# Optimization experiments

Measured on AMD Instinct MI355X. Metric: run time of the kernel, lower is better.

Reference implementation:

```python
import jax, jax.numpy as jnp
import numpy as np
from jax import lax

VOCAB, D, LAYERS, PAD = 10000, 200, 3, 3
B, S = 16, 512
SCALE = 0.05  # ~ torch uniform(-1/sqrt(200), 1/sqrt(200)) scale


def setup_inputs() -> dict:
    key = jax.random.key(0)
    ks = jax.random.split(key, 8)
    x = jax.random.randint(ks[0], (B, S), 0, VOCAB)
    emb = jax.random.normal(ks[1], (VOCAB, D), jnp.float32) * SCALE
    emb = emb.at[PAD].set(0.0)  # padding_idx=3 row is zeros
    w_ih = jax.random.normal(ks[2], (LAYERS, D, D), jnp.float32) * SCALE
    w_hh = jax.random.normal(ks[3], (LAYERS, D, D), jnp.float32) * SCALE
    b_ih = jax.random.normal(ks[4], (LAYERS, D), jnp.float32) * SCALE
    b_hh = jax.random.normal(ks[5], (LAYERS, D), jnp.float32) * SCALE
    fc_w = jax.random.normal(ks[6], (VOCAB, D), jnp.float32) * SCALE
    fc_b = jax.random.normal(ks[7], (VOCAB,), jnp.float32) * SCALE
    return {"x": x, "emb": emb, "w_ih": w_ih, "w_hh": w_hh,
            "b_ih": b_ih, "b_hh": b_hh, "fc_w": fc_w, "fc_b": fc_b}


def _rnn_forward(x, emb, w_ih, w_hh, b_ih, b_hh, fc_w, fc_b):
    h = emb[x]  # (B, S, D) embedding gather
    finals = []
    for l in range(LAYERS):
        # precompute input projection for the whole sequence (efficient GEMM)
        xw = jnp.einsum('bsd,hd->bsh', h, w_ih[l]) + b_ih[l] + b_hh[l]  # (B,S,D)
        w_hh_l_T = w_hh[l].T

        def step(h_prev, x_t):
            h_new = jnp.tanh(x_t + h_prev @ w_hh_l_T)
            return h_new, h_new

        h0 = jnp.zeros((x.shape[0], D), xw.dtype)
        h_last, outs = lax.scan(step, h0, jnp.swapaxes(xw, 0, 1))  # scan over time
        h = jnp.swapaxes(outs, 0, 1)  # (B, S, D)
        finals.append(h_last)
    hidden = jnp.stack(finals)  # (LAYERS, B, D) like torch RNN hidden
    logits = h @ fc_w.T + fc_b  # (B, S, VOCAB)
    return logits, hidden


def reference(x, emb, w_ih, w_hh, b_ih, b_hh, fc_w, fc_b):
    # forward always starts from zero hidden (source ignores the hidden arg)
    return _rnn_forward(x, emb, w_ih, w_hh, b_ih, b_hh, fc_w, fc_b)
```

## Files before the change

### kernel.cpp

```cpp
#include <hip/hip_runtime.h>
#include <hip/hip_bf16.h>

#define VOCAB 10000
#define D 200
#define NLAYERS 3
#define NB 16
#define NS 512
#define M 8192
#define KA 224
#define KB 232
#define NPADA 10120
#define NTILES_N 79

#define OFF_BUF0 0u
#define OFF_BUF1 6553600u
#define OFF_WT   13107200u
#define OFF_HBF  13587200u
#define OFF_FWB  17257216u
#define OFF_STG1 21952896u
#define WS_NEED  28506496u

typedef __bf16 bf16x8 __attribute__((ext_vector_type(8)));
typedef float  f32x4  __attribute__((ext_vector_type(4)));
typedef unsigned int u32x4 __attribute__((ext_vector_type(4)));

__global__ void k_embed(const int* __restrict__ x, const float* __restrict__ emb,
                        float* __restrict__ h0) {
    int i = blockIdx.x * blockDim.x + threadIdx.x;
    if (i < M * D) {
        int bs = i / D;
        int d  = i - bs * D;
        h0[i] = emb[(size_t)x[bs] * D + d];
    }
}

__global__ void k_wtrans(const float* __restrict__ w_ih, float* __restrict__ wt) {
    int i = blockIdx.x * blockDim.x + threadIdx.x;
    if (i < NLAYERS * D * D) {
        int l = i / (D * D);
        int r = i - l * D * D;
        int k = r / D;
        int n = r - k * D;
        wt[i] = w_ih[l * D * D + n * D + k];
    }
}

__global__ void k_fcwbf(const float* __restrict__ fc_w, __bf16* __restrict__ fwb) {
    int i = blockIdx.x * blockDim.x + threadIdx.x;
    if (i < NPADA * KB) {
        int n = i / KB;
        int k = i - n * KB;
        float v = (n < VOCAB && k < D) ? fc_w[(size_t)n * D + k] : 0.f;
        fwb[i] = (__bf16)v;
    }
}

__global__ void k_hbf2(const float* __restrict__ h, __bf16* __restrict__ hbf) {
    int i = blockIdx.x * blockDim.x + threadIdx.x;
    if (i < M * KA) {
        int m = i / KA;
        int k = i - m * KA;
        float v = (k < D) ? h[(size_t)m * D + k] : 0.f;
        hbf[i] = (__bf16)v;
    }
}

__global__ void k_zero(u32x4* __restrict__ p, int n4) {
    int i = blockIdx.x * blockDim.x + threadIdx.x;
    if (i < n4) p[i] = u32x4{0u, 0u, 0u, 0u};
}

__global__ void k_xw(const float* __restrict__ hin, const float* __restrict__ wt,
                     const float* __restrict__ b_ih, const float* __restrict__ b_hh,
                     float* __restrict__ xw) {
    int m0 = blockIdx.x * 32;
    int n  = threadIdx.x;
    if (n >= D) return;
    float bias = b_ih[n] + b_hh[n];
    for (int g = 0; g < 8; ++g) {
        const float* r0 = hin + (size_t)(m0 + g * 4) * D;
        float a0 = bias, a1 = bias, a2 = bias, a3 = bias;
        for (int k = 0; k < D; k += 4) {
            #pragma unroll
            for (int kk = 0; kk < 4; ++kk) {
                float w = wt[(k + kk) * D + n];
                float h0v = r0[k + kk];
                float h1v = r0[D + k + kk];
                float h2v = r0[2 * D + k + kk];
                float h3v = r0[3 * D + k + kk];
                a0 += h0v * w; a1 += h1v * w; a2 += h2v * w; a3 += h3v * w;
            }
        }
        size_t o = (size_t)(m0 + g * 4) * D + n;
        xw[o] = a0; xw[o + D] = a1; xw[o + 2 * D] = a2; xw[o + 3 * D] = a3;
    }
}

__device__ inline float fast_tanh(float x) {
    x = fminf(fmaxf(x, -15.f), 15.f);
    float e = __expf(2.f * x);
    return (e - 1.f) / (e + 1.f);
}

__global__ __attribute__((amdgpu_flat_work_group_size(512, 512),
                          amdgpu_waves_per_eu(2, 2)))
void k_scan_pipe(const float* __restrict__ whh_all,
                 const float* __restrict__ wih_all,
                 const float* __restrict__ b_ih,
                 const float* __restrict__ b_hh,
                 const float* __restrict__ xw0,
                 unsigned* __restrict__ stage0,
                 unsigned* __restrict__ stage1,
                 __bf16* __restrict__ hbf,
                 float* __restrict__ hidden) {
    __shared__ float hp0[208], hp1[208], hin[208];
    const int bid = blockIdx.x;
    const int l   = bid >> 4;
    const int b   = bid & 15;
    const int t   = threadIdx.x;
    const int q   = t >> 2, dg = t & 3;
    const bool act = (q < 100);
    const int  rr  = 2 * q + (dg & 1);
    const int  rrl = act ? rr : 0;
    const bool wlane = act && (dg < 2);
    const int  dstart = dg * 52;

    f32x4 wh[2][13], wi[2][13];
    #pragma unroll
    for (int j = 0; j < 2; ++j)
        #pragma unroll
        for (int i = 0; i < 13; ++i) {
            wh[j][i] = f32x4{0.f, 0.f, 0.f, 0.f};
            wi[j][i] = f32x4{0.f, 0.f, 0.f, 0.f};
        }
    if (act) {
        #pragma unroll
        for (int j = 0; j < 2; ++j) {
            const float* wr = whh_all + (size_t)l * D * D + (size_t)(2 * q + j) * D + dstart;
            #pragma unroll
            for (int i = 0; i < 11; ++i) wh[j][i] = *(const f32x4*)(wr + 4 * i);
            if (dg < 3) {
                wh[j][11] = *(const f32x4*)(wr + 44);
                wh[j][12] = *(const f32x4*)(wr + 48);
            }
        }
        if (l > 0) {
            #pragma unroll
            for (int j = 0; j < 2; ++j) {
                const float* wr = wih_all + (size_t)l * D * D + (size_t)(2 * q + j) * D + dstart;
                #pragma unroll
                for (int i = 0; i < 11; ++i) wi[j][i] = *(const f32x4*)(wr + 4 * i);
                if (dg < 3) {
                    wi[j][11] = *(const f32x4*)(wr + 44);
                    wi[j][12] = *(const f32x4*)(wr + 48);
                }
            }
        }
    }
    float bias = 0.f;
    if (l > 0 && act) bias = b_ih[l * D + rr] + b_hh[l * D + rr];

    if (t < 208) { hp0[t] = 0.f; hp1[t] = 0.f; hin[t] = 0.f; }
    __syncthreads();

    const float* xrow = xw0 + (size_t)b * NS * D;
    const unsigned* sin = (l == 1) ? stage0 + (size_t)b * NS * 200
                        : (l == 2) ? stage1 + (size_t)b * NS * 200 : nullptr;
    unsigned* sout = (l == 0) ? stage0 + (size_t)b * NS * 200
                   : (l == 1) ? stage1 + (size_t)b * NS * 200 : nullptr;

    float xv_next = (l == 0) ? xrow[rrl] : 0.f;
    float hlast = 0.f;
    const float* hi = hin + dstart;

    #pragma unroll 1
    for (int s = 0; s < NS; ++s) {
        float xv;
        if (l == 0) {
            xv = xv_next;
            const int sn = (s + 1 < NS) ? s + 1 : NS - 1;
            xv_next = xrow[(size_t)sn * D + rrl];
        } else {
            if (t < 200) {
                const unsigned* p = sin + (size_t)s * 200 + t;
                unsigned v;
                do {
                    v = __hip_atomic_load(p, __ATOMIC_RELAXED,
                                          __HIP_MEMORY_SCOPE_AGENT);
                } while (v == 0u);
                hin[t] = __builtin_bit_cast(float, ~v);
            }
            asm volatile("s_waitcnt lgkmcnt(0)" ::: "memory");
            __builtin_amdgcn_s_barrier();
            asm volatile("" ::: "memory");
            xv = bias;
        }
        const float* hr = ((s & 1) ? hp1 : hp0) + dstart;
        float* hw = (s & 1) ? hp0 : hp1;
        f32x4 ac0{0.f,0.f,0.f,0.f}, ac1{0.f,0.f,0.f,0.f};
        #pragma unroll
        for (int i = 0; i < 13; ++i) {
            f32x4 h4 = *(const f32x4*)(hr + 4 * i);
            ac0 += h4 * wh[0][i];
            ac1 += h4 * wh[1][i];
        }
        if (l > 0) {
            #pragma unroll
            for (int i = 0; i < 13; ++i) {
                f32x4 g4 = *(const f32x4*)(hi + 4 * i);
                ac0 += g4 * wi[0][i];
                ac1 += g4 * wi[1][i];
            }
        }
        float s0 = (ac0.x + ac0.y) + (ac0.z + ac0.w);
        float s1 = (ac1.x + ac1.y) + (ac1.z + ac1.w);
        s0 += __shfl_xor(s0, 1);  s0 += __shfl_xor(s0, 2);
        s1 += __shfl_xor(s1, 1);  s1 += __shfl_xor(s1, 2);
        float hn = fast_tanh(xv + ((dg & 1) ? s1 : s0));
        hlast = hn;
        if (wlane) {
            hw[rr] = hn;
            if (l < 2) {
                __hip_atomic_store(sout + (size_t)s * 200 + rr,
                                   ~__builtin_bit_cast(unsigned, hn),
                                   __ATOMIC_RELAXED, __HIP_MEMORY_SCOPE_AGENT);
            } else {
                hbf[((size_t)b * NS + s) * KA + rr] = (__bf16)hn;
            }
        }
        asm volatile("s_waitcnt lgkmcnt(0)" ::: "memory");
        __builtin_amdgcn_s_barrier();
        asm volatile("" ::: "memory");
    }
    if (wlane) hidden[(size_t)l * NB * D + b * D + rr] = hlast;
}

#define STEP(HR, HW, SIDX)                                                  \
    {                                                                       \
        float xv = xv_next;                                                 \
        int snext = (SIDX) + 1 < NS ? (SIDX) + 1 : NS - 1;                  \
        xv_next = xrow[(size_t)snext * D + rrl];                            \
        f32x4 ac0{0.f,0.f,0.f,0.f}, ac1{0.f,0.f,0.f,0.f};                   \
        _Pragma("unroll")                                                   \
        for (int i = 0; i < 13; ++i) {                                      \
            f32x4 h4 = *(const f32x4*)((HR) + 4 * i);                       \
            ac0 += h4 * w4[0][i];                                           \
            ac1 += h4 * w4[1][i];                                           \
        }                                                                   \
        float s0 = (ac0.x + ac0.y) + (ac0.z + ac0.w);                       \
        float s1 = (ac1.x + ac1.y) + (ac1.z + ac1.w);                       \
        s0 += __shfl_xor(s0, 1);  s0 += __shfl_xor(s0, 2);                  \
        s1 += __shfl_xor(s1, 1);  s1 += __shfl_xor(s1, 2);                  \
        float hn = fast_tanh(xv + ((dg & 1) ? s1 : s0));                    \
        hlast = hn;                                                         \
        if (wlane) {                                                        \
            (HW)[rr] = hn;                                                  \
            xrow[(size_t)(SIDX) * D + rr] = hn;                             \
        }                                                                   \
        __syncthreads();                                                    \
    }

__global__ __attribute__((amdgpu_flat_work_group_size(512, 512),
                          amdgpu_waves_per_eu(2, 2)))
void k_scan(const float* __restrict__ whh,
            float* __restrict__ io,
            float* __restrict__ hidden) {
    __shared__ float hp0[208], hp1[208];
    int t  = threadIdx.x;
    int b  = blockIdx.x;
    int q  = t >> 2;
    int dg = t & 3;
    const bool act = (q < 100);
    const int  rr  = 2 * q + (dg & 1);
    const int  rrl = act ? rr : 0;
    const bool wlane = act && (dg < 2);
    const int  dstart = dg * 52;

    f32x4 w4[2][13];
    #pragma unroll
    for (int j = 0; j < 2; ++j)
        #pragma unroll
        for (int i = 0; i < 13; ++i) w4[j][i] = f32x4{0.f, 0.f, 0.f, 0.f};
    if (act) {
        #pragma unroll
        for (int j = 0; j < 2; ++j) {
            const float* wr = whh + (size_t)(2 * q + j) * D + dstart;
            #pragma unroll
            for (int i = 0; i < 11; ++i) w4[j][i] = *(const f32x4*)(wr + 4 * i);
            if (dg < 3) {
                w4[j][11] = *(const f32x4*)(wr + 44);
                w4[j][12] = *(const f32x4*)(wr + 48);
            }
        }
    }
    if (t < 208) { hp0[t] = 0.f; hp1[t] = 0.f; }
    __syncthreads();

    float* xrow = io + (size_t)b * NS * D;
    const float* hr0 = hp0 + dstart;
    const float* hr1 = hp1 + dstart;
    float xv_next = xrow[rrl];
    float hlast = 0.f;

    #pragma unroll 1
    for (int s2 = 0; s2 < NS / 2; ++s2) {
        STEP(hr0, hp1, 2 * s2)
        STEP(hr1, hp0, 2 * s2 + 1)
    }
    if (wlane) hidden[b * D + rr] = hlast;
}

__global__ __launch_bounds__(256) void k_fc(const __bf16* __restrict__ A,
                                            const __bf16* __restrict__ Bw,
                                            const float* __restrict__ fc_b,
                                            float* __restrict__ Cout) {
    __shared__ __bf16 Bl[3840 * 8];
    int tid = threadIdx.x;
    int wg  = blockIdx.x;
    int mt  = wg / NTILES_N, nt = wg - mt * NTILES_N;
    int m0  = mt * 128, n0 = nt * 128;

    {
        const u32x4* src = (const u32x4*)(Bw + (size_t)n0 * KB);
        u32x4* dst = (u32x4*)Bl;
        u32x4 stg[15];
        #pragma unroll
        for (int it = 0; it < 15; ++it) stg[it] = src[tid + it * 256];
        #pragma unroll
        for (int it = 0; it < 15; ++it) dst[tid + it * 256] = stg[it];
    }
    __syncthreads();

    int lane = tid & 63, wv = tid >> 6;
    int wr = wv >> 1, wc = wv & 1;
    int lr = lane & 15, lq = lane >> 4;
    f32x4 acc[4][4] = {};
    #pragma unroll
    for (int ks = 0; ks < 7; ++ks) {
        bf16x8 af[4], bfr[4];
        #pragma unroll
        for (int i = 0; i < 4; ++i) {
            int arow = m0 + wr * 64 + i * 16 + lr;
            af[i] = *(const bf16x8*)(A + (size_t)arow * KA + (ks * 4 + lq) * 8);
            int brow = wc * 64 + i * 16 + lr;
            bfr[i] = *(const bf16x8*)(Bl + brow * KB + (ks * 4 + lq) * 8);
        }
        #pragma unroll
        for (int i = 0; i < 4; ++i) {
            #pragma unroll
            for (int j = 0; j < 4; ++j) {
                acc[i][j] = __builtin_amdgcn_mfma_f32_16x16x32_bf16(af[i], bfr[j],
                                                                   acc[i][j], 0, 0, 0);
            }
        }
    }
    #pragma unroll
    for (int j = 0; j < 4; ++j) {
        int col = n0 + wc * 64 + j * 16 + lr;
        if (col < VOCAB) {
            float bias = fc_b[col];
            #pragma unroll
            for (int i = 0; i < 4; ++i) {
                #pragma unroll
                for (int r = 0; r < 4; ++r) {
                    int row = m0 + wr * 64 + i * 16 + lq * 4 + r;
                    Cout[(size_t)row * VOCAB + col] = acc[i][j][r] + bias;
                }
            }
        }
    }
}

extern "C" void kernel_launch(void* const* d_in, const int* in_sizes, int n_in,
                              void* d_out, int out_size, void* d_ws, size_t ws_size,
                              hipStream_t stream) {
    const int*   x    = (const int*)  d_in[0];
    const float* emb  = (const float*)d_in[1];
    const float* w_ih = (const float*)d_in[2];
    const float* w_hh = (const float*)d_in[3];
    const float* b_ih = (const float*)d_in[4];
    const float* b_hh = (const float*)d_in[5];
    const float* fc_w = (const float*)d_in[6];
    const float* fc_b = (const float*)d_in[7];
    float* out    = (float*)d_out;
    float* hidden = out + (size_t)M * VOCAB;

    char* ws = (char*)d_ws;
    float*    buf0 = (float*)(ws + OFF_BUF0);
    float*    buf1 = (float*)(ws + OFF_BUF1);
    float*    wt   = (float*)(ws + OFF_WT);
    __bf16*   hbf  = (__bf16*)(ws + OFF_HBF);
    __bf16*   fwb  = (__bf16*)(ws + OFF_FWB);
    unsigned* stg0 = (unsigned*)(ws + OFF_BUF0);
    unsigned* stg1 = (unsigned*)(ws + OFF_STG1);

    k_embed <<<(M * D + 255) / 256, 256, 0, stream>>>(x, emb, buf0);
    k_wtrans<<<(NLAYERS * D * D + 255) / 256, 256, 0, stream>>>(w_ih, wt);
    k_fcwbf <<<(NPADA * KB + 255) / 256, 256, 0, stream>>>(fc_w, fwb);

    if (ws_size >= WS_NEED) {
        k_xw<<<M / 32, 256, 0, stream>>>(buf0, wt, b_ih, b_hh, buf1);
        const int nst4 = NB * NS * 200 / 4;
        const int nhb4 = M * KA * 2 / 16;
        k_zero<<<(nst4 + 255) / 256, 256, 0, stream>>>((u32x4*)stg0, nst4);
        k_zero<<<(nst4 + 255) / 256, 256, 0, stream>>>((u32x4*)stg1, nst4);
        k_zero<<<(nhb4 + 255) / 256, 256, 0, stream>>>((u32x4*)hbf, nhb4);
        k_scan_pipe<<<NB * NLAYERS, 512, 0, stream>>>(w_hh, w_ih, b_ih, b_hh,
                                                      buf1, stg0, stg1, hbf, hidden);
    } else {
        float* cur = buf0;
        float* nxt = buf1;
        for (int l = 0; l < NLAYERS; ++l) {
            k_xw  <<<M / 32, 256, 0, stream>>>(cur, wt + l * D * D,
                                               b_ih + l * D, b_hh + l * D, nxt);
            k_scan<<<NB, 512, 0, stream>>>(w_hh + (size_t)l * D * D, nxt,
                                           hidden + l * NB * D);
            float* tswap = cur; cur = nxt; nxt = tswap;
        }
        k_hbf2<<<(M * KA + 255) / 256, 256, 0, stream>>>(cur, hbf);
    }
    k_fc<<<64 * NTILES_N, 256, 0, stream>>>(hbf, fwb, fc_b, out);
}
```

Measured before the change: 866.7 us.

## Compute next layer's input projection in producer block, remove per-step input barrier

Each layer block now multiplies its freshly computed hidden state by the next layer's W_ih (plus bias) and publishes the projected value per row, instead of publishing raw h for the consumer to project. Consumer layers then only need one scalar per output row from the staging buffer, and they prefetch it one step ahead. This removes the separate LDS staging of the input vector and the extra barrier per timestep in consumer blocks. The cost is extra FMAs and registers in the producer's serial critical path. The loop also gains one extra iteration to drain the final projection.

```diff
diff --git a/kernel.cpp b/kernel.cpp
--- a/kernel.cpp
+++ b/kernel.cpp
@@ -109,11 +109,11 @@
                  const float* __restrict__ b_ih,
                  const float* __restrict__ b_hh,
                  const float* __restrict__ xw0,
-                 unsigned* __restrict__ stage0,
-                 unsigned* __restrict__ stage1,
+                 unsigned* __restrict__ cells1,
+                 unsigned* __restrict__ cells2,
                  __bf16* __restrict__ hbf,
                  float* __restrict__ hidden) {
-    __shared__ float hp0[208], hp1[208], hin[208];
+    __shared__ float hp0[208], hp1[208];
     const int bid = blockIdx.x;
     const int l   = bid >> 4;
     const int b   = bid & 15;
@@ -125,13 +125,13 @@
     const bool wlane = act && (dg < 2);
     const int  dstart = dg * 52;
 
-    f32x4 wh[2][13], wi[2][13];
+    f32x4 wh[2][13], wp[2][13];
     #pragma unroll
     for (int j = 0; j < 2; ++j)
         #pragma unroll
         for (int i = 0; i < 13; ++i) {
             wh[j][i] = f32x4{0.f, 0.f, 0.f, 0.f};
-            wi[j][i] = f32x4{0.f, 0.f, 0.f, 0.f};
+            wp[j][i] = f32x4{0.f, 0.f, 0.f, 0.f};
         }
     if (act) {
         #pragma unroll
@@ -144,95 +144,111 @@
                 wh[j][12] = *(const f32x4*)(wr + 48);
             }
         }
-        if (l > 0) {
+        if (l < 2) {
             #pragma unroll
             for (int j = 0; j < 2; ++j) {
-                const float* wr = wih_all + (size_t)l * D * D + (size_t)(2 * q + j) * D + dstart;
+                const float* wr = wih_all + (size_t)(l + 1) * D * D + (size_t)(2 * q + j) * D + dstart;
                 #pragma unroll
-                for (int i = 0; i < 11; ++i) wi[j][i] = *(const f32x4*)(wr + 4 * i);
+                for (int i = 0; i < 11; ++i) wp[j][i] = *(const f32x4*)(wr + 4 * i);
                 if (dg < 3) {
-                    wi[j][11] = *(const f32x4*)(wr + 44);
-                    wi[j][12] = *(const f32x4*)(wr + 48);
+                    wp[j][11] = *(const f32x4*)(wr + 44);
+                    wp[j][12] = *(const f32x4*)(wr + 48);
                 }
             }
         }
     }
-    float bias = 0.f;
-    if (l > 0 && act) bias = b_ih[l * D + rr] + b_hh[l * D + rr];
-
-    if (t < 208) { hp0[t] = 0.f; hp1[t] = 0.f; hin[t] = 0.f; }
+    float bN = 0.f;
+    if (l < 2 && act) bN = b_ih[(l + 1) * D + rr] + b_hh[(l + 1) * D + rr];
+
+    if (t < 208) { hp0[t] = 0.f; hp1[t] = 0.f; }
     __syncthreads();
 
     const float* xrow = xw0 + (size_t)b * NS * D;
-    const unsigned* sin = (l == 1) ? stage0 + (size_t)b * NS * 200
-                        : (l == 2) ? stage1 + (size_t)b * NS * 200 : nullptr;
-    unsigned* sout = (l == 0) ? stage0 + (size_t)b * NS * 200
-                   : (l == 1) ? stage1 + (size_t)b * NS * 200 : nullptr;
-
-    float xv_next = (l == 0) ? xrow[rrl] : 0.f;
-    float hlast = 0.f;
-    const float* hi = hin + dstart;
+    const unsigned* cin = (l == 1) ? cells1 + (size_t)b * NS * 200
+                        : (l == 2) ? cells2 + (size_t)b * NS * 200 : nullptr;
+    unsigned* cout_ = (l == 0) ? cells1 + (size_t)b * NS * 200
+                    : (l == 1) ? cells2 + (size_t)b * NS * 200 : nullptr;
+
+    float hn_prev = 0.f;
+    float xv_cur = 0.f;
+    unsigned v_cur = 0u;
+    if (l == 0) xv_cur = xrow[rrl];
 
     #pragma unroll 1
-    for (int s = 0; s < NS; ++s) {
-        float xv;
-        if (l == 0) {
-            xv = xv_next;
-            const int sn = (s + 1 < NS) ? s + 1 : NS - 1;
-            xv_next = xrow[(size_t)sn * D + rrl];
-        } else {
-            if (t < 200) {
-                const unsigned* p = sin + (size_t)s * 200 + t;
-                unsigned v;
-                do {
-                    v = __hip_atomic_load(p, __ATOMIC_RELAXED,
-                                          __HIP_MEMORY_SCOPE_AGENT);
-                } while (v == 0u);
-                hin[t] = __builtin_bit_cast(float, ~v);
-            }
-            asm volatile("s_waitcnt lgkmcnt(0)" ::: "memory");
-            __builtin_amdgcn_s_barrier();
-            asm volatile("" ::: "memory");
-            xv = bias;
-        }
-        const float* hr = ((s & 1) ? hp1 : hp0) + dstart;
-        float* hw = (s & 1) ? hp0 : hp1;
-        f32x4 ac0{0.f,0.f,0.f,0.f}, ac1{0.f,0.f,0.f,0.f};
-        #pragma unroll
-        for (int i = 0; i < 13; ++i) {
-            f32x4 h4 = *(const f32x4*)(hr + 4 * i);
-            ac0 += h4 * wh[0][i];
-            ac1 += h4 * wh[1][i];
-        }
-        if (l > 0) {
-            #pragma unroll
-            for (int i = 0; i < 13; ++i) {
-                f32x4 g4 = *(const f32x4*)(hi + 4 * i);
-                ac0 += g4 * wi[0][i];
-                ac1 += g4 * wi[1][i];
-            }
-        }
-        float s0 = (ac0.x + ac0.y) + (ac0.z + ac0.w);
-        float s1 = (ac1.x + ac1.y) + (ac1.z + ac1.w);
-        s0 += __shfl_xor(s0, 1);  s0 += __shfl_xor(s0, 2);
-        s1 += __shfl_xor(s1, 1);  s1 += __shfl_xor(s1, 2);
-        float hn = fast_tanh(xv + ((dg & 1) ? s1 : s0));
-        hlast = hn;
-        if (wlane) {
-            hw[rr] = hn;
-            if (l < 2) {
-                __hip_atomic_store(sout + (size_t)s * 200 + rr,
-                                   ~__builtin_bit_cast(unsigned, hn),
-                                   __ATOMIC_RELAXED, __HIP_MEMORY_SCOPE_AGENT);
-            } else {
-                hbf[((size_t)b * NS + s) * KA + rr] = (__bf16)hn;
-            }
-        }
+    for (int s = 0; s <= NS; ++s) {
+        float* hw = (s & 1) ? hp1 : hp0;
+        if (wlane) hw[rr] = hn_prev;
         asm volatile("s_waitcnt lgkmcnt(0)" ::: "memory");
         __builtin_amdgcn_s_barrier();
         asm volatile("" ::: "memory");
-    }
-    if (wlane) hidden[(size_t)l * NB * D + b * D + rr] = hlast;
+        const float* hr = hw + dstart;
+
+        f32x4 a0{0.f,0.f,0.f,0.f}, a1{0.f,0.f,0.f,0.f};
+        f32x4 p0{0.f,0.f,0.f,0.f}, p1{0.f,0.f,0.f,0.f};
+        if (l < 2) {
+            #pragma unroll
+            for (int i = 0; i < 13; ++i) {
+                f32x4 h4 = *(const f32x4*)(hr + 4 * i);
+                a0 += h4 * wh[0][i];
+                a1 += h4 * wh[1][i];
+                p0 += h4 * wp[0][i];
+                p1 += h4 * wp[1][i];
+            }
+        } else {
+            #pragma unroll
+            for (int i = 0; i < 13; ++i) {
+                f32x4 h4 = *(const f32x4*)(hr + 4 * i);
+                a0 += h4 * wh[0][i];
+                a1 += h4 * wh[1][i];
+            }
+        }
+
+        if (l < 2 && s >= 1) {
+            float t0 = (p0.x + p0.y) + (p0.z + p0.w);
+            float t1 = (p1.x + p1.y) + (p1.z + p1.w);
+            t0 += __shfl_xor(t0, 1);  t0 += __shfl_xor(t0, 2);
+            t1 += __shfl_xor(t1, 1);  t1 += __shfl_xor(t1, 2);
+            float xwp = ((dg & 1) ? t1 : t0) + bN;
+            if (wlane)
+                __hip_atomic_store(cout_ + (size_t)(s - 1) * 200 + rr,
+                                   ~__builtin_bit_cast(unsigned, xwp),
+                                   __ATOMIC_RELAXED, __HIP_MEMORY_SCOPE_AGENT);
+        }
+
+        if (s < NS) {
+            float xv;
+            if (l == 0) {
+                xv = xv_cur;
+            } else {
+                unsigned v = v_cur;
+                if (act) {
+                    while (v == 0u)
+                        v = __hip_atomic_load(cin + (size_t)s * 200 + rrl,
+                                              __ATOMIC_RELAXED,
+                                              __HIP_MEMORY_SCOPE_AGENT);
+                }
+                xv = __builtin_bit_cast(float, ~v);
+            }
+            const int sp = (s + 1 < NS) ? s + 1 : NS - 1;
+            if (l == 0) {
+                xv_cur = xrow[(size_t)sp * D + rrl];
+            } else {
+                v_cur = __hip_atomic_load(cin + (size_t)sp * 200 + rrl,
+                                          __ATOMIC_RELAXED,
+                                          __HIP_MEMORY_SCOPE_AGENT);
+            }
+
+            float s0 = (a0.x + a0.y) + (a0.z + a0.w);
+            float s1 = (a1.x + a1.y) + (a1.z + a1.w);
+            s0 += __shfl_xor(s0, 1);  s0 += __shfl_xor(s0, 2);
+            s1 += __shfl_xor(s1, 1);  s1 += __shfl_xor(s1, 2);
+            float hn = fast_tanh(xv + ((dg & 1) ? s1 : s0));
+            hn_prev = hn;
+            if (l == 2 && wlane)
+                hbf[((size_t)b * NS + s) * KA + rr] = (__bf16)hn;
+        }
+    }
+    if (wlane) hidden[(size_t)l * NB * D + b * D + rr] = hn_prev;
 }
 
 #define STEP(HR, HW, SIDX)                                                  \
```

After: 949.0 us. 9.5% more time.
